# Optimization experiments

Hardware: AMD Instinct MI355X
Metric: run time of the kernel (lower is better)

Reference implementation:

```python
import jax, jax.numpy as jnp
import numpy as np

# Problem sizes (packed acts shape = [B*T*(S+1), V])
B, T, S, V = 8, 400, 40, 512
BLANK = 0  # blank_label init kwarg
NEG_INF = jnp.float32(-1e30)


def setup_inputs() -> dict:
    key = jax.random.key(0)
    k1, k2 = jax.random.split(key)
    acts = jax.random.normal(k1, (B * T * (S + 1), V), dtype=jnp.float32)
    # labels are real (non-blank) symbols in [1, V)
    labels = jax.random.randint(k2, (B, S), 1, V).astype(jnp.int32)
    input_lengths = jnp.full((B,), T, dtype=jnp.int32)
    label_lengths = jnp.full((B,), S, dtype=jnp.int32)
    return {
        "acts": acts,
        "labels": labels,
        "input_lengths": input_lengths,
        "label_lengths": label_lengths,
    }


def _monotonic_rnnt_costs(acts, labels, input_lengths, label_lengths):
    # Module applies softmax internally -> work in log-prob space.
    lp = jax.nn.log_softmax(acts.reshape(B, T, S + 1, V), axis=-1)
    lp_blank = lp[..., BLANK]  # [B, T, S+1]
    # log P(y_{u+1} | t, u) for u in 0..S-1
    lp_label = jnp.take_along_axis(
        lp[:, :, :S, :], labels[:, None, :, None].astype(jnp.int32), axis=3
    )[..., 0]  # [B, T, S]

    # alpha[b, u] = log prob of emitting first u labels using frames processed so far.
    alpha0 = jnp.full((B, S + 1), NEG_INF, dtype=acts.dtype).at[:, 0].set(0.0)

    def step(alpha, xs):
        lpb_t, lpl_t = xs  # [B, S+1], [B, S]
        stay = alpha + lpb_t                 # emit blank: u unchanged
        move = alpha[:, :-1] + lpl_t         # emit label y_{u+1}: u -> u+1
        new = stay.at[:, 1:].set(jnp.logaddexp(stay[:, 1:], move))
        return new, new

    _, alphas = jax.lax.scan(
        step, alpha0, (jnp.swapaxes(lp_blank, 0, 1), jnp.swapaxes(lp_label, 0, 1))
    )  # alphas: [T, B, S+1], alphas[t] = alpha after t+1 frames

    b_idx = jnp.arange(B)
    costs = -alphas[input_lengths - 1, b_idx, label_lengths]  # [B]
    return costs


def reference(acts, labels, input_lengths, label_lengths):
    return _monotonic_rnnt_costs(acts, labels, input_lengths, label_lengths)
```

## Files before the change

kernel.cpp:

```cpp
#include <hip/hip_runtime.h>

#define TB 8
#define TT 400
#define TS 40
#define TV 512
#define SU (TS + 1)
#define NROWS (TB * TT * SU)
#define SS 8
#define NSS (TT / SS)
#define NW (SS + 1)
#define GRP 5
#define NGRP (NSS / GRP)
#define NEG_INF (-1.0e30f)
#define INV_LN2 1.44269504088896341f
#define LN2 0.69314718055994531f

__device__ __forceinline__ float wave_shr1(float x) {
    return __int_as_float(
        __builtin_amdgcn_update_dpp(0, __float_as_int(x), 0x138, 0xf, 0xf, true));
}

__device__ __forceinline__ float lse2(float a, float c) {
    const float mx = fmaxf(a, c), mn = fminf(a, c);
    return mx + __builtin_amdgcn_logf(1.0f + __builtin_amdgcn_exp2f(mn - mx));
}

__global__ __launch_bounds__(256) void rowlse_kernel(
    const float* __restrict__ acts, const int* __restrict__ labels,
    float* __restrict__ lp_blank, float* __restrict__ lp_label)
{
    const int wave = threadIdx.x >> 6;
    const int lane = threadIdx.x & 63;
    const int row  = blockIdx.x * 4 + wave;

    const float* rp = acts + (size_t)row * TV;
    float4 a = *(const float4*)(rp + lane * 8);
    float4 b = *(const float4*)(rp + lane * 8 + 4);

    float m = fmaxf(fmaxf(fmaxf(a.x, a.y), fmaxf(a.z, a.w)),
                    fmaxf(fmaxf(b.x, b.y), fmaxf(b.z, b.w)));
#pragma unroll
    for (int off = 1; off < 64; off <<= 1) m = fmaxf(m, __shfl_xor(m, off));

    float s = __expf(a.x - m) + __expf(a.y - m) + __expf(a.z - m) + __expf(a.w - m)
            + __expf(b.x - m) + __expf(b.y - m) + __expf(b.z - m) + __expf(b.w - m);
#pragma unroll
    for (int off = 1; off < 64; off <<= 1) s += __shfl_xor(s, off);

    const float logZ = m + logf(s);

    if (lane == 0) {
        const int u  = row % SU;
        const int bt = row / SU;
        lp_blank[row] = (a.x - logZ) * INV_LN2;
        if (u < TS) {
            const int b_idx = bt / TT;
            const int col   = labels[b_idx * TS + u];
            lp_label[bt * TS + u] = (rp[col] - logZ) * INV_LN2;
        }
    }
}

__global__ __launch_bounds__(256) void compose_kernel(
    const float* __restrict__ lp_blank, const float* __restrict__ lp_label,
    float* __restrict__ W)
{
    const int wv   = blockIdx.x * 4 + (threadIdx.x >> 6);
    const int lane = threadIdx.x & 63;
    const int b  = wv / NSS;
    const int s  = wv - b * NSS;
    const int t0 = s * SS;
    const int uu = (lane <= TS) ? lane : TS;
    const bool have_l = (lane >= 1 && lane <= TS);

    const float* pb = lp_blank + ((size_t)b * TT + t0) * SU + uu;
    const float* pl = lp_label + ((size_t)b * TT + t0) * TS + (have_l ? lane - 1 : 0);

    float bm[SS], lm[SS];
#pragma unroll
    for (int m = 0; m < SS; ++m) {
        bm[m] = pb[m * SU];
        float lv = pl[m * TS];
        lm[m] = have_l ? lv : NEG_INF;
    }

    float E[NW];
    E[0] = 0.0f;
#pragma unroll
    for (int j = 1; j < NW; ++j) E[j] = NEG_INF;

#pragma unroll
    for (int m = 0; m < SS; ++m) {
#pragma unroll
        for (int jj = 0; jj < NW - 1; ++jj) {
            const int j = (NW - 1) - jj;
            if (j <= m + 1)
                E[j] = lse2(E[j] + bm[m], wave_shr1(E[j - 1]) + lm[m]);
        }
        E[0] += bm[m];
    }

    if (lane <= TS) {
        float* wp = W + (((size_t)b * NSS + s) * NW) * SU + lane;
#pragma unroll
        for (int j = 0; j < NW; ++j)
            wp[j * SU] = (lane >= j) ? E[j] : NEG_INF;
    }
}

__global__ __launch_bounds__(64) void scan_kernel(
    const float* __restrict__ W,
    const float* __restrict__ lp_blank, const float* __restrict__ lp_label,
    const int* __restrict__ input_lengths, const int* __restrict__ label_lengths,
    float* __restrict__ out)
{
    const int b = blockIdx.x;
    const int u = threadIdx.x;

    const int inlen  = input_lengths[b];
    const int lablen = label_lengths[b];
    const int rr     = inlen & (SS - 1);
    const int s_part = inlen >> 3;
    const int s_cap  = (rr == 0) ? s_part - 1 : -1;

    const int uu = (u <= TS) ? u : TS;
    const int ul = (u >= 1 && u <= TS) ? (u - 1) : 0;
    const bool u_dead = (u == 0 || u > TS);
    const float* wbase = W + ((size_t)b * NSS * NW) * SU + uu;

    float alpha = (u == 0) ? 0.0f : NEG_INF;
    float saved = NEG_INF;

    float wA[GRP * NW], wB[GRP * NW];

#define LOADG(BUF, G) { \
    _Pragma("unroll") \
    for (int ss = 0; ss < GRP; ++ss) { \
        _Pragma("unroll") \
        for (int j = 0; j < NW; ++j) \
            (BUF)[ss * NW + j] = wbase[((size_t)((((G) * GRP + ss) * NW) + j)) * SU]; \
    } }

#define COMPG(BUF, G) { \
    _Pragma("unroll") \
    for (int ss = 0; ss < GRP; ++ss) { \
        const int s = (G) * GRP + ss; \
        if (rr && s == s_part) {  \
            float a2 = alpha; \
            _Pragma("unroll") \
            for (int q = 0; q < SS - 1; ++q) { \
                if (q < rr) { \
                    const int t = SS * s_part + q; \
                    const float pbv = lp_blank[((size_t)b * TT + t) * SU + uu]; \
                    float plv = lp_label[((size_t)b * TT + t) * TS + ul]; \
                    plv = u_dead ? NEG_INF : plv; \
                    const float prev = wave_shr1(a2); \
                    a2 = lse2(a2 + pbv, prev + plv); \
                } \
            } \
            saved = a2; \
        } \
        const float s1 = wave_shr1(alpha), s2 = wave_shr1(s1); \
        const float s3 = wave_shr1(s2),    s4 = wave_shr1(s3); \
        const float s5 = wave_shr1(s4),    s6 = wave_shr1(s5); \
        const float s7 = wave_shr1(s6),    s8 = wave_shr1(s7); \
        const float T0 = alpha + (BUF)[ss * NW + 0]; \
        const float T1 = s1 + (BUF)[ss * NW + 1]; \
        const float T2 = s2 + (BUF)[ss * NW + 2]; \
        const float T3 = s3 + (BUF)[ss * NW + 3]; \
        const float T4 = s4 + (BUF)[ss * NW + 4]; \
        const float T5 = s5 + (BUF)[ss * NW + 5]; \
        const float T6 = s6 + (BUF)[ss * NW + 6]; \
        const float T7 = s7 + (BUF)[ss * NW + 7]; \
        const float T8 = s8 + (BUF)[ss * NW + 8]; \
        const float M = fmaxf(fmaxf(fmaxf(fmaxf(T0, T1), fmaxf(T2, T3)), \
                                    fmaxf(fmaxf(T4, T5), fmaxf(T6, T7))), T8); \
        const float sm = ((__builtin_amdgcn_exp2f(T0 - M) + __builtin_amdgcn_exp2f(T1 - M)) \
                       +  (__builtin_amdgcn_exp2f(T2 - M) + __builtin_amdgcn_exp2f(T3 - M))) \
                       + ((__builtin_amdgcn_exp2f(T4 - M) + __builtin_amdgcn_exp2f(T5 - M)) \
                       +  (__builtin_amdgcn_exp2f(T6 - M) + __builtin_amdgcn_exp2f(T7 - M))) \
                       +   __builtin_amdgcn_exp2f(T8 - M); \
        alpha = M + __builtin_amdgcn_logf(sm); \
        if (s == s_cap) saved = alpha; \
    } }

    LOADG(wA, 0);
    for (int i = 0; i < 4; ++i) {
        const int g0 = 2 * i;
        LOADG(wB, g0 + 1);
        COMPG(wA, g0);
        LOADG(wA, g0 + 2);
        COMPG(wB, g0 + 1);
    }
    LOADG(wB, 9);
    COMPG(wA, 8);
    COMPG(wB, 9);

#undef LOADG
#undef COMPG

    const float cost_alpha = __shfl(saved, lablen);
    if (u == 0) out[b] = -cost_alpha * LN2;
}

extern "C" void kernel_launch(void* const* d_in, const int* in_sizes, int n_in,
                              void* d_out, int out_size, void* d_ws, size_t ws_size,
                              hipStream_t stream) {
    const float* acts          = (const float*)d_in[0];
    const int*   labels        = (const int*)d_in[1];
    const int*   input_lengths = (const int*)d_in[2];
    const int*   label_lengths = (const int*)d_in[3];
    float* out = (float*)d_out;

    float* lp_blank = (float*)d_ws;
    float* lp_label = lp_blank + NROWS;
    float* W        = lp_label + (size_t)TB * TT * TS;

    rowlse_kernel<<<NROWS / 4, 256, 0, stream>>>(acts, labels, lp_blank, lp_label);
    compose_kernel<<<TB * NSS / 4, 256, 0, stream>>>(lp_blank, lp_label, W);
    scan_kernel<<<TB, 64, 0, stream>>>(W, lp_blank, lp_label,
                                       input_lengths, label_lengths, out);
}
```

Baseline: 56.58 us.

## Fuse compose and scan into one per-batch kernel with LDS staging

Merges the compose and scan kernels into a single 1024-thread block per batch element. Composed 8-step transfer matrices now live in shared memory instead of a global workspace. The second half of the compositions is computed by the other 15 waves while wave 0 scans the first half, overlapping the two stages. This removes one kernel launch and the global round trip for W, at the cost of only 8 blocks doing all compose work and extra block-level barriers.

```diff
diff --git a/kernel.cpp b/kernel.cpp
--- a/kernel.cpp
+++ b/kernel.cpp
@@ -8,9 +8,8 @@
 #define NROWS (TB * TT * SU)
 #define SS 8
 #define NSS (TT / SS)
+#define HALF (NSS / 2)
 #define NW (SS + 1)
-#define GRP 5
-#define NGRP (NSS / GRP)
 #define NEG_INF (-1.0e30f)
 #define INV_LN2 1.44269504088896341f
 #define LN2 0.69314718055994531f
@@ -61,14 +60,10 @@
     }
 }
 
-__global__ __launch_bounds__(256) void compose_kernel(
+__device__ __forceinline__ void compose8_regs(
     const float* __restrict__ lp_blank, const float* __restrict__ lp_label,
-    float* __restrict__ W)
+    int b, int s, int lane, float* E)
 {
-    const int wv   = blockIdx.x * 4 + (threadIdx.x >> 6);
-    const int lane = threadIdx.x & 63;
-    const int b  = wv / NSS;
-    const int s  = wv - b * NSS;
     const int t0 = s * SS;
     const int uu = (lane <= TS) ? lane : TS;
     const bool have_l = (lane >= 1 && lane <= TS);
@@ -84,7 +79,6 @@
         lm[m] = have_l ? lv : NEG_INF;
     }
 
-    float E[NW];
     E[0] = 0.0f;
 #pragma unroll
     for (int j = 1; j < NW; ++j) E[j] = NEG_INF;
@@ -99,108 +93,127 @@
         }
         E[0] += bm[m];
     }
-
+}
+
+__device__ __forceinline__ void store_E(const float* E, int lane, float* dst) {
     if (lane <= TS) {
-        float* wp = W + (((size_t)b * NSS + s) * NW) * SU + lane;
 #pragma unroll
         for (int j = 0; j < NW; ++j)
-            wp[j * SU] = (lane >= j) ? E[j] : NEG_INF;
-    }
-}
-
-__global__ __launch_bounds__(64) void scan_kernel(
-    const float* __restrict__ W,
+            dst[j * SU + lane] = (lane >= j) ? E[j] : NEG_INF;
+    }
+}
+
+__global__ __launch_bounds__(1024) void tail_kernel(
     const float* __restrict__ lp_blank, const float* __restrict__ lp_label,
     const int* __restrict__ input_lengths, const int* __restrict__ label_lengths,
     float* __restrict__ out)
 {
-    const int b = blockIdx.x;
-    const int u = threadIdx.x;
+    __shared__ float Wlds[HALF][NW][SU];
+    const int b    = blockIdx.x;
+    const int wv   = threadIdx.x >> 6;
+    const int lane = threadIdx.x & 63;
 
     const int inlen  = input_lengths[b];
     const int lablen = label_lengths[b];
     const int rr     = inlen & (SS - 1);
     const int s_part = inlen >> 3;
     const int s_cap  = (rr == 0) ? s_part - 1 : -1;
-
-    const int uu = (u <= TS) ? u : TS;
-    const int ul = (u >= 1 && u <= TS) ? (u - 1) : 0;
-    const bool u_dead = (u == 0 || u > TS);
-    const float* wbase = W + ((size_t)b * NSS * NW) * SU + uu;
-
-    float alpha = (u == 0) ? 0.0f : NEG_INF;
+    const int uu = (lane <= TS) ? lane : TS;
+    const int ul = (lane >= 1 && lane <= TS) ? (lane - 1) : 0;
+    const bool u_dead = (lane == 0 || lane > TS);
+    float alpha = (lane == 0) ? 0.0f : NEG_INF;
     float saved = NEG_INF;
 
-    float wA[GRP * NW], wB[GRP * NW];
-
-#define LOADG(BUF, G) { \
+    for (int s = wv; s < HALF; s += 16) {
+        float E[NW];
+        compose8_regs(lp_blank, lp_label, b, s, lane, E);
+        store_E(E, lane, &Wlds[s][0][0]);
+    }
+    __syncthreads();
+
+#define LOADW(BUF, ss) { \
     _Pragma("unroll") \
-    for (int ss = 0; ss < GRP; ++ss) { \
+    for (int j = 0; j < NW; ++j) (BUF)[j] = Wlds[(ss)][j][uu]; }
+
+#define STEP(BUF, GS) { \
+    const int gs = (GS); \
+    if (rr && gs == s_part) {    \
+        float a2 = alpha; \
         _Pragma("unroll") \
-        for (int j = 0; j < NW; ++j) \
-            (BUF)[ss * NW + j] = wbase[((size_t)((((G) * GRP + ss) * NW) + j)) * SU]; \
-    } }
-
-#define COMPG(BUF, G) { \
-    _Pragma("unroll") \
-    for (int ss = 0; ss < GRP; ++ss) { \
-        const int s = (G) * GRP + ss; \
-        if (rr && s == s_part) {  \
-            float a2 = alpha; \
-            _Pragma("unroll") \
-            for (int q = 0; q < SS - 1; ++q) { \
-                if (q < rr) { \
-                    const int t = SS * s_part + q; \
-                    const float pbv = lp_blank[((size_t)b * TT + t) * SU + uu]; \
-                    float plv = lp_label[((size_t)b * TT + t) * TS + ul]; \
-                    plv = u_dead ? NEG_INF : plv; \
-                    const float prev = wave_shr1(a2); \
-                    a2 = lse2(a2 + pbv, prev + plv); \
-                } \
+        for (int q = 0; q < SS - 1; ++q) { \
+            if (q < rr) { \
+                const int t = SS * s_part + q; \
+                const float pbv = lp_blank[((size_t)b * TT + t) * SU + uu]; \
+                float plv = lp_label[((size_t)b * TT + t) * TS + ul]; \
+                plv = u_dead ? NEG_INF : plv; \
+                a2 = lse2(a2 + pbv, wave_shr1(a2) + plv); \
             } \
-            saved = a2; \
         } \
-        const float s1 = wave_shr1(alpha), s2 = wave_shr1(s1); \
-        const float s3 = wave_shr1(s2),    s4 = wave_shr1(s3); \
-        const float s5 = wave_shr1(s4),    s6 = wave_shr1(s5); \
-        const float s7 = wave_shr1(s6),    s8 = wave_shr1(s7); \
-        const float T0 = alpha + (BUF)[ss * NW + 0]; \
-        const float T1 = s1 + (BUF)[ss * NW + 1]; \
-        const float T2 = s2 + (BUF)[ss * NW + 2]; \
-        const float T3 = s3 + (BUF)[ss * NW + 3]; \
-        const float T4 = s4 + (BUF)[ss * NW + 4]; \
-        const float T5 = s5 + (BUF)[ss * NW + 5]; \
-        const float T6 = s6 + (BUF)[ss * NW + 6]; \
-        const float T7 = s7 + (BUF)[ss * NW + 7]; \
-        const float T8 = s8 + (BUF)[ss * NW + 8]; \
-        const float M = fmaxf(fmaxf(fmaxf(fmaxf(T0, T1), fmaxf(T2, T3)), \
-                                    fmaxf(fmaxf(T4, T5), fmaxf(T6, T7))), T8); \
-        const float sm = ((__builtin_amdgcn_exp2f(T0 - M) + __builtin_amdgcn_exp2f(T1 - M)) \
-                       +  (__builtin_amdgcn_exp2f(T2 - M) + __builtin_amdgcn_exp2f(T3 - M))) \
-                       + ((__builtin_amdgcn_exp2f(T4 - M) + __builtin_amdgcn_exp2f(T5 - M)) \
-                       +  (__builtin_amdgcn_exp2f(T6 - M) + __builtin_amdgcn_exp2f(T7 - M))) \
-                       +   __builtin_amdgcn_exp2f(T8 - M); \
-        alpha = M + __builtin_amdgcn_logf(sm); \
-        if (s == s_cap) saved = alpha; \
-    } }
-
-    LOADG(wA, 0);
-    for (int i = 0; i < 4; ++i) {
-        const int g0 = 2 * i;
-        LOADG(wB, g0 + 1);
-        COMPG(wA, g0);
-        LOADG(wA, g0 + 2);
-        COMPG(wB, g0 + 1);
-    }
-    LOADG(wB, 9);
-    COMPG(wA, 8);
-    COMPG(wB, 9);
-
-#undef LOADG
-#undef COMPG
-
-    const float cost_alpha = __shfl(saved, lablen);
-    if (u == 0) out[b] = -cost_alpha * LN2;
+        saved = a2; \
+    } \
+    const float s1 = wave_shr1(alpha), s2 = wave_shr1(s1); \
+    const float s3 = wave_shr1(s2),    s4 = wave_shr1(s3); \
+    const float s5 = wave_shr1(s4),    s6 = wave_shr1(s5); \
+    const float s7 = wave_shr1(s6),    s8 = wave_shr1(s7); \
+    const float T0 = alpha + (BUF)[0]; \
+    const float T1 = s1 + (BUF)[1]; \
+    const float T2 = s2 + (BUF)[2]; \
+    const float T3 = s3 + (BUF)[3]; \
+    const float T4 = s4 + (BUF)[4]; \
+    const float T5 = s5 + (BUF)[5]; \
+    const float T6 = s6 + (BUF)[6]; \
+    const float T7 = s7 + (BUF)[7]; \
+    const float T8 = s8 + (BUF)[8]; \
+    const float M = fmaxf(fmaxf(fmaxf(fmaxf(T0, T1), fmaxf(T2, T3)), \
+                                fmaxf(fmaxf(T4, T5), fmaxf(T6, T7))), T8); \
+    const float sm = ((__builtin_amdgcn_exp2f(T0 - M) + __builtin_amdgcn_exp2f(T1 - M)) \
+                   +  (__builtin_amdgcn_exp2f(T2 - M) + __builtin_amdgcn_exp2f(T3 - M))) \
+                   + ((__builtin_amdgcn_exp2f(T4 - M) + __builtin_amdgcn_exp2f(T5 - M)) \
+                   +  (__builtin_amdgcn_exp2f(T6 - M) + __builtin_amdgcn_exp2f(T7 - M))) \
+                   +   __builtin_amdgcn_exp2f(T8 - M); \
+    alpha = M + __builtin_amdgcn_logf(sm); \
+    if (gs == s_cap) saved = alpha; }
+
+#define SCAN_HALF(BASE) { \
+    float wA[NW], wB[NW]; \
+    LOADW(wA, 0); \
+    for (int i = 0; i < 12; ++i) { \
+        const int ss0 = 2 * i; \
+        LOADW(wB, ss0 + 1); \
+        STEP(wA, (BASE) + ss0); \
+        LOADW(wA, ss0 + 2); \
+        STEP(wB, (BASE) + ss0 + 1); \
+    } \
+    STEP(wA, (BASE) + HALF - 1); }
+
+    float Er0[NW], Er1[NW];
+    int nm = 0, sm0 = 0, sm1 = 0;
+    if (wv == 0) {
+        SCAN_HALF(0);
+    } else {
+        for (int s = HALF + (wv - 1); s < NSS; s += 15) {
+            if (nm == 0) { compose8_regs(lp_blank, lp_label, b, s, lane, Er0); sm0 = s; }
+            else         { compose8_regs(lp_blank, lp_label, b, s, lane, Er1); sm1 = s; }
+            ++nm;
+        }
+    }
+    __syncthreads();
+
+    if (wv != 0) {
+        if (nm >= 1) store_E(Er0, lane, &Wlds[sm0 - HALF][0][0]);
+        if (nm >= 2) store_E(Er1, lane, &Wlds[sm1 - HALF][0][0]);
+    }
+    __syncthreads();
+
+    if (wv == 0) {
+        SCAN_HALF(HALF);
+        const float cost_alpha = __shfl(saved, lablen);
+        if (lane == 0) out[b] = -cost_alpha * LN2;
+    }
+
+#undef LOADW
+#undef STEP
+#undef SCAN_HALF
 }
 
 extern "C" void kernel_launch(void* const* d_in, const int* in_sizes, int n_in,
@@ -214,10 +227,8 @@
 
     float* lp_blank = (float*)d_ws;
     float* lp_label = lp_blank + NROWS;
-    float* W        = lp_label + (size_t)TB * TT * TS;
 
     rowlse_kernel<<<NROWS / 4, 256, 0, stream>>>(acts, labels, lp_blank, lp_label);
-    compose_kernel<<<TB * NSS / 4, 256, 0, stream>>>(lp_blank, lp_label, W);
-    scan_kernel<<<TB, 64, 0, stream>>>(W, lp_blank, lp_label,
-                                       input_lengths, label_lengths, out);
-}
+    tail_kernel<<<TB, 1024, 0, stream>>>(lp_blank, lp_label,
+                                         input_lengths, label_lengths, out);
+}
```

After: 60.87 us. 7.6% more time.

## Fuse row log-softmax and segment composition into one block-per-segment kernel

Applied to the files above, without the earlier changes.

Merges the per-row log-softmax kernel and the segment composition kernel into a single kernel where each 1024-thread block computes all rows of one 8-frame segment, stages blank/label log-probs in shared memory, then one wave composes the segment transfer matrix. This removes a kernel launch and the global-memory round trip for lp values feeding composition. It trades away the very fine-grained row parallelism (many small blocks) for 400 large blocks, which may reduce load balance and memory-latency hiding, and leaves 15 waves idle during composition.

```diff
diff --git a/kernel.cpp b/kernel.cpp
--- a/kernel.cpp
+++ b/kernel.cpp
@@ -10,7 +10,6 @@
 #define NSS (TT / SS)
 #define NW (SS + 1)
 #define GRP 5
-#define NGRP (NSS / GRP)
 #define NEG_INF (-1.0e30f)
 #define INV_LN2 1.44269504088896341f
 #define LN2 0.69314718055994531f
@@ -25,86 +24,89 @@
     return mx + __builtin_amdgcn_logf(1.0f + __builtin_amdgcn_exp2f(mn - mx));
 }
 
-__global__ __launch_bounds__(256) void rowlse_kernel(
+__global__ __launch_bounds__(1024) void lse_compose_kernel(
     const float* __restrict__ acts, const int* __restrict__ labels,
-    float* __restrict__ lp_blank, float* __restrict__ lp_label)
-{
-    const int wave = threadIdx.x >> 6;
-    const int lane = threadIdx.x & 63;
-    const int row  = blockIdx.x * 4 + wave;
-
-    const float* rp = acts + (size_t)row * TV;
-    float4 a = *(const float4*)(rp + lane * 8);
-    float4 b = *(const float4*)(rp + lane * 8 + 4);
-
-    float m = fmaxf(fmaxf(fmaxf(a.x, a.y), fmaxf(a.z, a.w)),
-                    fmaxf(fmaxf(b.x, b.y), fmaxf(b.z, b.w)));
-#pragma unroll
-    for (int off = 1; off < 64; off <<= 1) m = fmaxf(m, __shfl_xor(m, off));
-
-    float s = __expf(a.x - m) + __expf(a.y - m) + __expf(a.z - m) + __expf(a.w - m)
-            + __expf(b.x - m) + __expf(b.y - m) + __expf(b.z - m) + __expf(b.w - m);
-#pragma unroll
-    for (int off = 1; off < 64; off <<= 1) s += __shfl_xor(s, off);
-
-    const float logZ = m + logf(s);
-
-    if (lane == 0) {
-        const int u  = row % SU;
-        const int bt = row / SU;
-        lp_blank[row] = (a.x - logZ) * INV_LN2;
-        if (u < TS) {
-            const int b_idx = bt / TT;
-            const int col   = labels[b_idx * TS + u];
-            lp_label[bt * TS + u] = (rp[col] - logZ) * INV_LN2;
-        }
-    }
-}
-
-__global__ __launch_bounds__(256) void compose_kernel(
-    const float* __restrict__ lp_blank, const float* __restrict__ lp_label,
+    float* __restrict__ lp_blank, float* __restrict__ lp_label,
     float* __restrict__ W)
 {
-    const int wv   = blockIdx.x * 4 + (threadIdx.x >> 6);
+    __shared__ float lds_b[SS][SU];
+    __shared__ float lds_l[SS][TS];
+    const int blk  = blockIdx.x;
+    const int b    = blk / NSS;
+    const int s    = blk - b * NSS;
+    const int wv   = threadIdx.x >> 6;
     const int lane = threadIdx.x & 63;
-    const int b  = wv / NSS;
-    const int s  = wv - b * NSS;
-    const int t0 = s * SS;
-    const int uu = (lane <= TS) ? lane : TS;
-    const bool have_l = (lane >= 1 && lane <= TS);
-
-    const float* pb = lp_blank + ((size_t)b * TT + t0) * SU + uu;
-    const float* pl = lp_label + ((size_t)b * TT + t0) * TS + (have_l ? lane - 1 : 0);
-
-    float bm[SS], lm[SS];
-#pragma unroll
-    for (int m = 0; m < SS; ++m) {
-        bm[m] = pb[m * SU];
-        float lv = pl[m * TS];
-        lm[m] = have_l ? lv : NEG_INF;
+    const int t0   = s * SS;
+
+    for (int r = wv; r < SS * SU; r += 16) {
+        const int t  = r / SU;
+        const int u  = r - t * SU;
+        const int bt = b * TT + t0 + t;
+        const size_t row = (size_t)bt * SU + u;
+
+        const float* rp = acts + row * TV;
+        float4 a  = *(const float4*)(rp + lane * 8);
+        float4 bv = *(const float4*)(rp + lane * 8 + 4);
+
+        float m = fmaxf(fmaxf(fmaxf(a.x, a.y), fmaxf(a.z, a.w)),
+                        fmaxf(fmaxf(bv.x, bv.y), fmaxf(bv.z, bv.w)));
+#pragma unroll
+        for (int off = 1; off < 64; off <<= 1) m = fmaxf(m, __shfl_xor(m, off));
+
+        float sum = __expf(a.x-m)+__expf(a.y-m)+__expf(a.z-m)+__expf(a.w-m)
+                  + __expf(bv.x-m)+__expf(bv.y-m)+__expf(bv.z-m)+__expf(bv.w-m);
+#pragma unroll
+        for (int off = 1; off < 64; off <<= 1) sum += __shfl_xor(sum, off);
+
+        const float logZ = m + logf(sum);
+
+        if (lane == 0) {
+            const float vb = (a.x - logZ) * INV_LN2;
+            lds_b[t][u]   = vb;
+            lp_blank[row] = vb;
+            if (u < TS) {
+                const int col  = labels[b * TS + u];
+                const float vl = (rp[col] - logZ) * INV_LN2;
+                lds_l[t][u] = vl;
+                lp_label[bt * TS + u] = vl;
+            }
+        }
     }
-
-    float E[NW];
-    E[0] = 0.0f;
-#pragma unroll
-    for (int j = 1; j < NW; ++j) E[j] = NEG_INF;
-
-#pragma unroll
-    for (int m = 0; m < SS; ++m) {
-#pragma unroll
-        for (int jj = 0; jj < NW - 1; ++jj) {
-            const int j = (NW - 1) - jj;
-            if (j <= m + 1)
-                E[j] = lse2(E[j] + bm[m], wave_shr1(E[j - 1]) + lm[m]);
-        }
-        E[0] += bm[m];
-    }
-
-    if (lane <= TS) {
-        float* wp = W + (((size_t)b * NSS + s) * NW) * SU + lane;
-#pragma unroll
-        for (int j = 0; j < NW; ++j)
-            wp[j * SU] = (lane >= j) ? E[j] : NEG_INF;
+    __syncthreads();
+
+    if (wv == 0) {
+        const int uu = (lane <= TS) ? lane : TS;
+        const bool have_l = (lane >= 1 && lane <= TS);
+
+        float bm[SS], lm[SS];
+#pragma unroll
+        for (int m = 0; m < SS; ++m) {
+            bm[m] = lds_b[m][uu];
+            lm[m] = have_l ? lds_l[m][lane - 1] : NEG_INF;
+        }
+
+        float E[NW];
+        E[0] = 0.0f;
+#pragma unroll
+        for (int j = 1; j < NW; ++j) E[j] = NEG_INF;
+
+#pragma unroll
+        for (int m = 0; m < SS; ++m) {
+#pragma unroll
+            for (int jj = 0; jj < NW - 1; ++jj) {
+                const int j = (NW - 1) - jj;
+                if (j <= m + 1)
+                    E[j] = lse2(E[j] + bm[m], wave_shr1(E[j - 1]) + lm[m]);
+            }
+            E[0] += bm[m];
+        }
+
+        if (lane <= TS) {
+            float* wp = W + (((size_t)b * NSS + s) * NW) * SU + lane;
+#pragma unroll
+            for (int j = 0; j < NW; ++j)
+                wp[j * SU] = (lane >= j) ? E[j] : NEG_INF;
+        }
     }
 }
 
@@ -216,8 +218,8 @@
     float* lp_label = lp_blank + NROWS;
     float* W        = lp_label + (size_t)TB * TT * TS;
 
-    rowlse_kernel<<<NROWS / 4, 256, 0, stream>>>(acts, labels, lp_blank, lp_label);
-    compose_kernel<<<TB * NSS / 4, 256, 0, stream>>>(lp_blank, lp_label, W);
+    lse_compose_kernel<<<TB * NSS, 1024, 0, stream>>>(acts, labels,
+                                                      lp_blank, lp_label, W);
     scan_kernel<<<TB, 64, 0, stream>>>(W, lp_blank, lp_label,
                                        input_lengths, label_lengths, out);
 }
```

Result: slower. 63.97 us (+13.1%).
